# Optimization experiments

Measured on AMD Instinct MI355X. Metric: run time of the kernel, lower is better.

## Reference

```python
import jax, jax.numpy as jnp
import numpy as np

E = 8          # num_experts
K = 2          # top_k
CAPF = 1.25    # capacity_factor
DIM = 512
HID = 2048     # int(dim * mlp_ratio)


def setup_inputs() -> dict:
    key = jax.random.key(0)
    ks = jax.random.split(key, 5)
    s = 0.02
    x = jax.random.normal(ks[0], (8, 2048, DIM), jnp.float32)
    Wr = jax.random.normal(ks[1], (E, DIM), jnp.float32) * s          # router weight (no bias)
    W1 = jax.random.normal(ks[2], (E, HID, DIM), jnp.float32) * s     # fc1 weights per expert
    b1 = jnp.zeros((E, HID), jnp.float32)
    W2 = jax.random.normal(ks[3], (E, DIM, HID), jnp.float32) * s     # fc2 weights per expert
    b2 = jnp.zeros((E, DIM), jnp.float32)
    return {"x": x, "Wr": Wr, "W1": W1, "b1": b1, "W2": W2, "b2": b2}


def _capacity_keep(top_w, top_idx, cap):
    """For each (slot, expert), keep only the `cap` highest-weight tokens.
    top_w, top_idx: [T, K]. Returns bool keep mask [T, K]."""
    def per_slot(w, idx):
        order = jnp.argsort(-w)                       # tokens sorted by weight desc
        idx_sorted = idx[order]                       # [T] expert id in sorted order
        oh = jax.nn.one_hot(idx_sorted, E, dtype=jnp.int32)
        rank = jnp.cumsum(oh, axis=0) - 1             # rank within each expert
        r = jnp.take_along_axis(rank, idx_sorted[:, None], axis=1)[:, 0]
        keep_sorted = r < cap
        return jnp.zeros(w.shape[0], bool).at[order].set(keep_sorted)
    return jax.vmap(per_slot, in_axes=(1, 1), out_axes=1)(top_w, top_idx)


def reference(x, Wr, W1, b1, W2, b2):
    b, n, d = x.shape
    T = b * n
    flat = x.reshape(T, d)

    # Router: softmax in fp32 then cast back
    logits = flat @ Wr.T                                            # [T, E]
    probs = jax.nn.softmax(logits.astype(jnp.float32), axis=-1).astype(flat.dtype)
    top_w, top_idx = jax.lax.top_k(probs, K)                        # [T, K]
    top_w = top_w / (jnp.sum(top_w, axis=-1, keepdims=True) + 1e-8)

    # Capacity-limited drop, then renormalize
    cap = max(1, int(CAPF * T * K / E))
    keep = _capacity_keep(top_w, top_idx, cap)
    top_w = jnp.where(keep, top_w, 0.0)
    top_w = top_w / jnp.clip(jnp.sum(top_w, axis=-1, keepdims=True), 1e-8, None)

    # Combine weight per (token, expert): scatter-add top_w into dense [T, E]
    rows = jnp.arange(T)[:, None]
    w_te = jnp.zeros((T, E), flat.dtype).at[rows, top_idx].add(top_w)

    # Per-expert MLP, weighted combine (w_te is 0 for unassigned/dropped pairs)
    out = jnp.zeros_like(flat)
    for e in range(E):
        h = jax.nn.gelu(flat @ W1[e].T + b1[e], approximate=False)  # [T, HID]
        y = h @ W2[e].T + b2[e]                                     # [T, D]
        out = out + w_te[:, e:e + 1] * y

    # Load-balancing aux loss
    load = jnp.sum(w_te, axis=0) / T
    importance = probs.mean(0)
    aux = jnp.sum(importance * load * float(E))
    return out.reshape(b, n, d), aux
```

## Files before the change

### kernel.cpp

```cpp
#include <hip/hip_runtime.h>
#include <hip/hip_bf16.h>
#include <math.h>

#define DIM 512
#define HID 2048
#define NE  8
#define CSTRIDE 32
#define CVTB 1024

typedef __attribute__((ext_vector_type(8))) short short8;
typedef __attribute__((ext_vector_type(4))) float f32x4;
typedef unsigned short ushort_t;

static __device__ __forceinline__ ushort_t f2bf(float f) {
    unsigned int x = __builtin_bit_cast(unsigned int, f);
    unsigned int lsb = (x >> 16) & 1u;
    x += 0x7fffu + lsb;
    return (ushort_t)(x >> 16);
}
static __device__ __forceinline__ float bf2f(ushort_t u) {
    unsigned int x = ((unsigned int)u) << 16;
    return __builtin_bit_cast(float, x);
}

static __device__ __forceinline__ float fast_gelu(float v) {
    float z = v * fmaf(0.071354816f, v * v, 1.5957691f);
    return v * __builtin_amdgcn_rcpf(1.f + __expf(-z));
}

static __device__ __forceinline__ void gld16(const void* g, void* l) {
    __builtin_amdgcn_global_load_lds(
        (const __attribute__((address_space(1))) void*)g,
        (__attribute__((address_space(3))) void*)l,
        16, 0, 0);
}

__global__ __launch_bounds__(256) void k_init(
    const float* __restrict__ W1, ushort_t* __restrict__ W1b, int n1,
    const float* __restrict__ W2, ushort_t* __restrict__ W2b, int n2,
    const float* __restrict__ x, const float* __restrict__ Wr,
    ushort_t* __restrict__ xb, float* __restrict__ probs,
    int* __restrict__ tidx, float* __restrict__ tw, int T)
{
    if (blockIdx.x < CVTB) {
        int i = blockIdx.x * 256 + threadIdx.x;
        int stride = CVTB * 256;
        int n4a = n1 >> 2, n4b = n2 >> 2;
        for (int j = i; j < n4a; j += stride) {
            float4 v = ((const float4*)W1)[j];
            ushort4 o;
            o.x = f2bf(v.x); o.y = f2bf(v.y); o.z = f2bf(v.z); o.w = f2bf(v.w);
            ((ushort4*)W1b)[j] = o;
        }
        for (int j = i; j < n4b; j += stride) {
            float4 v = ((const float4*)W2)[j];
            ushort4 o;
            o.x = f2bf(v.x); o.y = f2bf(v.y); o.z = f2bf(v.z); o.w = f2bf(v.w);
            ((ushort4*)W2b)[j] = o;
        }
        return;
    }
    int lane = threadIdx.x & 63;
    int t = (blockIdx.x - CVTB) * 4 + (threadIdx.x >> 6);
    if (t >= T) return;
    const float* xr = x + (size_t)t * DIM;
    double acc[NE];
#pragma unroll
    for (int e = 0; e < NE; e++) acc[e] = 0.0;
    for (int i = lane; i < DIM; i += 64) {
        float xv = xr[i];
        xb[(size_t)t * DIM + i] = f2bf(xv);
        double xd = (double)xv;
#pragma unroll
        for (int e = 0; e < NE; e++) acc[e] += xd * (double)Wr[e * DIM + i];
    }
#pragma unroll
    for (int e = 0; e < NE; e++) {
#pragma unroll
        for (int off = 32; off > 0; off >>= 1) acc[e] += __shfl_xor(acc[e], off);
    }
    double mx = acc[0];
#pragma unroll
    for (int e = 1; e < NE; e++) mx = fmax(mx, acc[e]);
    double p[NE], sum = 0.0;
#pragma unroll
    for (int e = 0; e < NE; e++) { p[e] = exp(acc[e] - mx); sum += p[e]; }
    float pr[NE];
#pragma unroll
    for (int e = 0; e < NE; e++) pr[e] = (float)(p[e] / sum);
    if (lane < NE) probs[(size_t)t * NE + lane] = pr[lane];
    if (lane == 0) {
        int i1 = 0; float b1v = pr[0];
#pragma unroll
        for (int e = 1; e < NE; e++) if (pr[e] > b1v) { b1v = pr[e]; i1 = e; }
        int i2 = -1; float b2v = -1.f;
#pragma unroll
        for (int e = 0; e < NE; e++) if (e != i1 && pr[e] > b2v) { b2v = pr[e]; i2 = e; }
        float s2 = b1v + b2v + 1e-8f;
        tidx[t * 2] = i1; tidx[t * 2 + 1] = i2;
        tw[t * 2] = b1v / s2; tw[t * 2 + 1] = b2v / s2;
    }
}

__global__ __launch_bounds__(256) void k_hist(const int* __restrict__ tidx,
                                              int* __restrict__ cnt, int T) {
    __shared__ int h[16];
    if (threadIdx.x < 16) h[threadIdx.x] = 0;
    __syncthreads();
    int stride = gridDim.x * blockDim.x;
    for (int t = blockIdx.x * blockDim.x + threadIdx.x; t < T; t += stride) {
        atomicAdd(&h[tidx[t * 2]], 1);
        atomicAdd(&h[8 + tidx[t * 2 + 1]], 1);
    }
    __syncthreads();
    if (threadIdx.x < 16 && h[threadIdx.x] != 0)
        atomicAdd(&cnt[threadIdx.x * CSTRIDE], h[threadIdx.x]);
}

__global__ __launch_bounds__(256) void k_post(const int* __restrict__ tidx,
        const float* __restrict__ tw, const int* __restrict__ cnt,
        const float* __restrict__ probs, int* __restrict__ lcnt,
        int* __restrict__ ltok, int* __restrict__ pos, float* __restrict__ tw2,
        float* __restrict__ partial, int T, int cap, int capM)
{
    __shared__ int h[NE];
    __shared__ int base[NE];
    __shared__ float red[256 * 16];
    if (threadIdx.x < NE) h[threadIdx.x] = 0;
    __syncthreads();
    int t = blockIdx.x * blockDim.x + threadIdx.x;
    float wkn[2] = {0.f, 0.f};
    int myE[2] = {-1, -1};
    int myp[2] = {0, 0};
    if (t < T) {
        float wk[2]; int es[2];
#pragma unroll
        for (int s = 0; s < 2; s++) {
            int e = tidx[t * 2 + s];
            float w = tw[t * 2 + s];
            es[s] = e; wk[s] = w;
            if (cnt[(s * NE + e) * CSTRIDE] > cap) {
                int rank = 0;
                for (int t2 = 0; t2 < T; t2++) {
                    if (tidx[t2 * 2 + s] == e) {
                        float w2 = tw[t2 * 2 + s];
                        if (w2 > w || (w2 == w && t2 < t)) rank++;
                    }
                }
                if (rank >= cap) wk[s] = 0.f;
            }
        }
        float denom = fmaxf(wk[0] + wk[1], 1e-8f);
#pragma unroll
        for (int s = 0; s < 2; s++) {
            wkn[s] = wk[s] / denom;
            tw2[t * 2 + s] = wkn[s];
            if (wkn[s] != 0.f) {
                myE[s] = es[s];
                myp[s] = atomicAdd(&h[es[s]], 1);
            }
        }
    }
    __syncthreads();
    if (threadIdx.x < NE)
        base[threadIdx.x] = (h[threadIdx.x] != 0)
            ? atomicAdd(&lcnt[threadIdx.x * CSTRIDE], h[threadIdx.x]) : 0;
    __syncthreads();
    float imp[NE], ld[NE];
#pragma unroll
    for (int e = 0; e < NE; e++) { imp[e] = 0.f; ld[e] = 0.f; }
    if (t < T) {
#pragma unroll
        for (int s = 0; s < 2; s++) {
            if (myE[s] >= 0) {
                int p = base[myE[s]] + myp[s];
                ltok[myE[s] * capM + p] = t;
                pos[t * 2 + s] = (myE[s] << 20) | p;
                ld[myE[s]] += wkn[s];
            } else {
                pos[t * 2 + s] = -1;
            }
        }
#pragma unroll
        for (int e = 0; e < NE; e++) imp[e] = probs[(size_t)t * NE + e];
    }
#pragma unroll
    for (int e = 0; e < NE; e++) {
        red[threadIdx.x * 16 + e] = imp[e];
        red[threadIdx.x * 16 + 8 + e] = ld[e];
    }
    __syncthreads();
    for (int off = 128; off > 0; off >>= 1) {
        if (threadIdx.x < off) {
#pragma unroll
            for (int j = 0; j < 16; j++)
                red[threadIdx.x * 16 + j] += red[(threadIdx.x + off) * 16 + j];
        }
        __syncthreads();
    }
    if (threadIdx.x < 16) partial[blockIdx.x * 16 + threadIdx.x] = red[threadIdx.x];
}

__global__ void k_tail(const int* __restrict__ lcnt, int* __restrict__ loff,
                       const float* __restrict__ partial, float* __restrict__ outaux,
                       int nb, int T)
{
    __shared__ float s[16];
    if (threadIdx.x == 0) {
        int o = 0;
        for (int e = 0; e < NE; e++) {
            loff[e] = o;
            o += ((lcnt[e * CSTRIDE] + 127) >> 7) << 7;
        }
        loff[NE] = o;
    }
    if (threadIdx.x < 16) {
        float a = 0.f;
        for (int b = 0; b < nb; b++) a += partial[b * 16 + threadIdx.x];
        s[threadIdx.x] = a;
    }
    __syncthreads();
    if (threadIdx.x == 0) {
        float invT = 1.f / (float)T;
        float aux = 0.f;
        for (int e = 0; e < NE; e++)
            aux += (s[e] * invT) * (s[8 + e] * invT) * (float)NE;
        outaux[0] = aux;
    }
}

__global__ __launch_bounds__(256, 2) void k_fc1(
    const ushort_t* __restrict__ xb, const ushort_t* __restrict__ W1b,
    const float* __restrict__ b1, const int* __restrict__ lcnt,
    const int* __restrict__ loff, const int* __restrict__ ltok,
    ushort_t* __restrict__ hbuf, int capM)
{
    int bx = blockIdx.x;
    int e  = bx & 7;
    int r  = bx >> 3;
    int mt = r >> 4;
    int nt = r & 15;
    int cnt = lcnt[e * CSTRIDE];
    if (cnt > capM) cnt = capM;
    int m0 = mt * 128;
    if (m0 >= cnt) return;
    int n0 = nt * 128;
    const int* toks = ltok + e * capM;
    int hrow0 = loff[e] + m0;
    const ushort_t* Bsrc = W1b + (size_t)e * HID * DIM;

    __shared__ char smem[65536];
    char* As0 = smem;          char* Bs0 = smem + 16384;
    char* As1 = smem + 32768;  char* Bs1 = smem + 49152;

    int tid = threadIdx.x;
    int wave = tid >> 6, lane = tid & 63;
    int wm = wave >> 1, wn = wave & 1;

    const char* aSrc[4]; const char* bSrc[4]; int ldst[4];
#pragma unroll
    for (int i = 0; i < 4; i++) {
        int c = tid + 256 * i;
        int row = c >> 3, cc = c & 7;
        int scc = cc ^ (row & 7);
        int gr = m0 + row;
        int tok = toks[gr < cnt ? gr : (cnt - 1)];
        aSrc[i] = (const char*)(xb + (size_t)tok * DIM + scc * 8);
        bSrc[i] = (const char*)(Bsrc + (size_t)(n0 + row) * DIM + scc * 8);
        ldst[i] = (i * 256 + wave * 64) * 16;
    }

    f32x4 acc[4][4];
#pragma unroll
    for (int a = 0; a < 4; a++)
#pragma unroll
        for (int b = 0; b < 4; b++) acc[a][b] = (f32x4){0.f, 0.f, 0.f, 0.f};

    int aRow = wm * 64 + (lane & 15);
    int bRow = wn * 64 + (lane & 15);
    int kq = lane >> 4;
    int swz0 = (kq ^ (lane & 7)) << 4;
    int swz1 = ((4 + kq) ^ (lane & 7)) << 4;
    int aoff[2] = { aRow * 128 + swz0, aRow * 128 + swz1 };
    int boff[2] = { bRow * 128 + swz0, bRow * 128 + swz1 };

    auto STAGE = [&](int kofs, char* A, char* B) {
#pragma unroll
        for (int i = 0; i < 4; i++) {
            gld16(aSrc[i] + kofs, A + ldst[i]);
            gld16(bSrc[i] + kofs, B + ldst[i]);
        }
    };
    auto COMPUTE = [&](const char* A, const char* B) {
#pragma unroll
        for (int kk = 0; kk < 2; kk++) {
            short8 af[4], bfr[4];
#pragma unroll
            for (int mf = 0; mf < 4; mf++)
                af[mf] = *(const short8*)(A + aoff[kk] + mf * 2048);
#pragma unroll
            for (int nf = 0; nf < 4; nf++)
                bfr[nf] = *(const short8*)(B + boff[kk] + nf * 2048);
#pragma unroll
            for (int mf = 0; mf < 4; mf++)
#pragma unroll
                for (int nf = 0; nf < 4; nf++)
                    acc[mf][nf] = __builtin_amdgcn_mfma_f32_16x16x32_bf16(bfr[nf], af[mf], acc[mf][nf], 0, 0, 0);
        }
    };

    const int NT = DIM / 64;
    STAGE(0, As0, Bs0);
#pragma unroll
    for (int t = 0; t < NT; t++) {
        char* Ac = (t & 1) ? As1 : As0;
        char* Bc = (t & 1) ? Bs1 : Bs0;
        if (t + 1 < NT) {
            STAGE((t + 1) * 128, (t & 1) ? As0 : As1, (t & 1) ? Bs0 : Bs1);
            asm volatile("s_waitcnt vmcnt(8)" ::: "memory");
        } else {
            asm volatile("s_waitcnt vmcnt(0)" ::: "memory");
        }
        __builtin_amdgcn_s_barrier();
        __builtin_amdgcn_sched_barrier(0);
        COMPUTE(Ac, Bc);
        __builtin_amdgcn_sched_barrier(0);
        __builtin_amdgcn_s_barrier();
    }

    const float* b1e = b1 + e * HID;
    int mlocal = wm * 64 + (lane & 15);
    int nbase0 = n0 + wn * 64 + (lane >> 4) * 4;
#pragma unroll
    for (int mf = 0; mf < 4; mf++) {
        int mrow = mlocal + mf * 16;
        bool valid = (m0 + mrow) < cnt;
        ushort_t* dst = hbuf + (size_t)(hrow0 + mrow) * HID;
#pragma unroll
        for (int nf = 0; nf < 4; nf++) {
            int nc = nbase0 + nf * 16;
            float4 bias4 = *(const float4*)(b1e + nc);
            ushort4 o;
            o.x = f2bf(fast_gelu(acc[mf][nf][0] + bias4.x));
            o.y = f2bf(fast_gelu(acc[mf][nf][1] + bias4.y));
            o.z = f2bf(fast_gelu(acc[mf][nf][2] + bias4.z));
            o.w = f2bf(fast_gelu(acc[mf][nf][3] + bias4.w));
            if (valid) *(ushort4*)(dst + nc) = o;
        }
    }
}

__global__ __launch_bounds__(256, 2) void k_fc2(
    const ushort_t* __restrict__ hbuf, const ushort_t* __restrict__ W2b,
    const float* __restrict__ b2, const int* __restrict__ lcnt,
    const int* __restrict__ loff, ushort_t* __restrict__ ybuf, int capM)
{
    int bx = blockIdx.x;
    int e  = bx & 7;
    int r  = bx >> 3;
    int mt = r >> 2;
    int nt = r & 3;
    int cnt = lcnt[e * CSTRIDE];
    if (cnt > capM) cnt = capM;
    int m0 = mt * 128;
    if (m0 >= cnt) return;
    int n0 = nt * 128;
    int hrow0 = loff[e] + m0;
    const ushort_t* Bsrc = W2b + (size_t)e * DIM * HID;

    __shared__ char smem[65536];
    char* As0 = smem;          char* Bs0 = smem + 16384;
    char* As1 = smem + 32768;  char* Bs1 = smem + 49152;

    int tid = threadIdx.x;
    int wave = tid >> 6, lane = tid & 63;
    int wm = wave >> 1, wn = wave & 1;

    const char* aSrc[4]; const char* bSrc[4]; int ldst[4];
#pragma unroll
    for (int i = 0; i < 4; i++) {
        int c = tid + 256 * i;
        int row = c >> 3, cc = c & 7;
        int scc = cc ^ (row & 7);
        aSrc[i] = (const char*)(hbuf + (size_t)(hrow0 + row) * HID + scc * 8);
        bSrc[i] = (const char*)(Bsrc + (size_t)(n0 + row) * HID + scc * 8);
        ldst[i] = (i * 256 + wave * 64) * 16;
    }

    f32x4 acc[4][4];
#pragma unroll
    for (int a = 0; a < 4; a++)
#pragma unroll
        for (int b = 0; b < 4; b++) acc[a][b] = (f32x4){0.f, 0.f, 0.f, 0.f};

    int aRow = wm * 64 + (lane & 15);
    int bRow = wn * 64 + (lane & 15);
    int kq = lane >> 4;
    int swz0 = (kq ^ (lane & 7)) << 4;
    int swz1 = ((4 + kq) ^ (lane & 7)) << 4;
    int aoff[2] = { aRow * 128 + swz0, aRow * 128 + swz1 };
    int boff[2] = { bRow * 128 + swz0, bRow * 128 + swz1 };

    auto STAGE = [&](int kofs, char* A, char* B) {
#pragma unroll
        for (int i = 0; i < 4; i++) {
            gld16(aSrc[i] + kofs, A + ldst[i]);
            gld16(bSrc[i] + kofs, B + ldst[i]);
        }
    };
    auto COMPUTE = [&](const char* A, const char* B) {
#pragma unroll
        for (int kk = 0; kk < 2; kk++) {
            short8 af[4], bfr[4];
#pragma unroll
            for (int mf = 0; mf < 4; mf++)
                af[mf] = *(const short8*)(A + aoff[kk] + mf * 2048);
#pragma unroll
            for (int nf = 0; nf < 4; nf++)
                bfr[nf] = *(const short8*)(B + boff[kk] + nf * 2048);
#pragma unroll
            for (int mf = 0; mf < 4; mf++)
#pragma unroll
                for (int nf = 0; nf < 4; nf++)
                    acc[mf][nf] = __builtin_amdgcn_mfma_f32_16x16x32_bf16(bfr[nf], af[mf], acc[mf][nf], 0, 0, 0);
        }
    };

    const int NT = HID / 64;
    STAGE(0, As0, Bs0);
#pragma unroll
    for (int t = 0; t < NT; t++) {
        char* Ac = (t & 1) ? As1 : As0;
        char* Bc = (t & 1) ? Bs1 : Bs0;
        if (t + 1 < NT) {
            STAGE((t + 1) * 128, (t & 1) ? As0 : As1, (t & 1) ? Bs0 : Bs1);
            asm volatile("s_waitcnt vmcnt(8)" ::: "memory");
        } else {
            asm volatile("s_waitcnt vmcnt(0)" ::: "memory");
        }
        __builtin_amdgcn_s_barrier();
        __builtin_amdgcn_sched_barrier(0);
        COMPUTE(Ac, Bc);
        __builtin_amdgcn_sched_barrier(0);
        __builtin_amdgcn_s_barrier();
    }

    const float* b2e = b2 + e * DIM;
    int mlocal = wm * 64 + (lane & 15);
    int nbase0 = n0 + wn * 64 + (lane >> 4) * 4;
#pragma unroll
    for (int mf = 0; mf < 4; mf++) {
        int mrow = mlocal + mf * 16;
        bool valid = (m0 + mrow) < cnt;
        ushort_t* dst = ybuf + (size_t)(hrow0 + mrow) * DIM;
#pragma unroll
        for (int nf = 0; nf < 4; nf++) {
            int nc = nbase0 + nf * 16;
            float4 bias4 = *(const float4*)(b2e + nc);
            ushort4 o;
            o.x = f2bf(acc[mf][nf][0] + bias4.x);
            o.y = f2bf(acc[mf][nf][1] + bias4.y);
            o.z = f2bf(acc[mf][nf][2] + bias4.z);
            o.w = f2bf(acc[mf][nf][3] + bias4.w);
            if (valid) *(ushort4*)(dst + nc) = o;
        }
    }
}

__global__ __launch_bounds__(256) void k_comb(const ushort_t* __restrict__ ybuf,
    const float* __restrict__ tw2, const int* __restrict__ pos,
    const int* __restrict__ loff, float* __restrict__ out, int T, int capM)
{
    int wv = threadIdx.x >> 6, lane = threadIdx.x & 63;
    int t = blockIdx.x * 4 + wv;
    if (t >= T) return;
    float o[8];
#pragma unroll
    for (int j = 0; j < 8; j++) o[j] = 0.f;
#pragma unroll
    for (int s = 0; s < 2; s++) {
        int pk = pos[t * 2 + s];
        if (pk >= 0) {
            float w = tw2[t * 2 + s];
            int e = pk >> 20, p = pk & 0xFFFFF;
            int row = loff[e] + p;
            short8 y = *(const short8*)(ybuf + (size_t)row * DIM + lane * 8);
#pragma unroll
            for (int j = 0; j < 8; j++) o[j] += w * bf2f((ushort_t)y[j]);
        }
    }
    float4* dst = (float4*)(out + (size_t)t * DIM + lane * 8);
    dst[0] = (float4){o[0], o[1], o[2], o[3]};
    dst[1] = (float4){o[4], o[5], o[6], o[7]};
}

extern "C" void kernel_launch(void* const* d_in, const int* in_sizes, int n_in,
                              void* d_out, int out_size, void* d_ws, size_t ws_size,
                              hipStream_t stream)
{
    const float* x  = (const float*)d_in[0];
    const float* Wr = (const float*)d_in[1];
    const float* W1 = (const float*)d_in[2];
    const float* b1 = (const float*)d_in[3];
    const float* W2 = (const float*)d_in[4];
    const float* b2 = (const float*)d_in[5];
    float* out = (float*)d_out;

    int T = in_sizes[0] / DIM;
    int cap = (int)(1.25 * (double)T * 2.0 / 8.0);
    if (cap < 1) cap = 1;
    int capM = 2 * cap; if (capM > T) capM = T;
    int mtmax = (capM + 127) / 128;
    int nposts = (T + 255) / 256;

    char* w = (char*)d_ws;
    size_t off = 0;
    auto alloc = [&](size_t bytes) {
        char* p = w + off;
        off = (off + bytes + 255) & ~(size_t)255;
        return p;
    };
    size_t ybrows = (size_t)T * 2 + NE * 128;
    size_t ybbytes = ybrows * DIM * 2;
    ushort_t* ybuf = (ushort_t*)w;
    ushort_t* xb   = (ushort_t*)alloc((size_t)T * DIM * 2);
    ushort_t* W1b  = (ushort_t*)alloc((size_t)NE * HID * DIM * 2);
    if (off < ybbytes) off = (ybbytes + 255) & ~(size_t)255;
    ushort_t* W2b  = (ushort_t*)alloc((size_t)NE * DIM * HID * 2);
    ushort_t* hbuf = (ushort_t*)alloc(ybrows * HID * 2);
    float* probs   = (float*)alloc((size_t)T * NE * 4);
    int*   tidx    = (int*)alloc((size_t)T * 2 * 4);
    float* tw      = (float*)alloc((size_t)T * 2 * 4);
    float* tw2     = (float*)alloc((size_t)T * 2 * 4);
    int*   pos     = (int*)alloc((size_t)T * 2 * 4);
    int*   cnt     = (int*)alloc(16 * CSTRIDE * 4);
    int*   lcnt    = (int*)alloc(NE * CSTRIDE * 4);
    int*   loff    = (int*)alloc((NE + 1) * 4);
    int*   ltok    = (int*)alloc((size_t)NE * capM * 4);
    float* partial = (float*)alloc((size_t)nposts * 16 * 4);

    (void)hipMemsetAsync(cnt, 0, 16 * CSTRIDE * 4, stream);
    (void)hipMemsetAsync(lcnt, 0, NE * CSTRIDE * 4, stream);

    int nrb = (T + 3) / 4;
    k_init<<<CVTB + nrb, 256, 0, stream>>>(W1, W1b, NE * HID * DIM,
                                           W2, W2b, NE * DIM * HID,
                                           x, Wr, xb, probs, tidx, tw, T);
    k_hist<<<64, 256, 0, stream>>>(tidx, cnt, T);
    k_post<<<nposts, 256, 0, stream>>>(tidx, tw, cnt, probs, lcnt, ltok, pos, tw2,
                                       partial, T, cap, capM);
    k_tail<<<1, 64, 0, stream>>>(lcnt, loff, partial, out + (size_t)T * DIM, nposts, T);

    k_fc1<<<NE * mtmax * (HID / 128), 256, 0, stream>>>(
        xb, W1b, b1, lcnt, loff, ltok, hbuf, capM);
    k_fc2<<<NE * mtmax * (DIM / 128), 256, 0, stream>>>(
        hbuf, W2b, b2, lcnt, loff, ybuf, capM);
    k_comb<<<(T + 3) / 4, 256, 0, stream>>>(ybuf, tw2, pos, loff, out, T, capM);
}
```

Baseline: 267.3 us.

## Enlarge expert GEMM tiles to 256x256 with 8 waves and interleaved MFMA phases

Moves the fc1 and fc2 grouped GEMMs from 128x128 tiles with 4 waves to 256x256 tiles with 8 waves. Each wave now holds 128x64 accumulators, and the kernels use 128KB of dynamic LDS for double buffering. The inner loop is split into four phases separated by barriers, with s_setprio raised around the MFMA bursts so waves interleave LDS reads and matrix math. Expert segment padding grows to 256 rows. The aim is more operand reuse per LDS load, at the cost of higher register pressure, fewer blocks per CU, and more padded wasted rows for small expert counts.

```diff
diff --git a/kernel.cpp b/kernel.cpp
--- a/kernel.cpp
+++ b/kernel.cpp
@@ -34,6 +34,19 @@
         (__attribute__((address_space(3))) void*)l,
         16, 0, 0);
 }
+
+#define LOADB4(Bb, KK) { _Pragma("unroll") \
+    for (int nf = 0; nf < 4; nf++) \
+        bfr[nf] = *(const short8*)((Bb) + boff[KK] + nf * 2048); }
+#define LOADA4(Ab, KK, MH) { _Pragma("unroll") \
+    for (int j = 0; j < 4; j++) \
+        af[j] = *(const short8*)((Ab) + aoff[KK] + ((MH) * 4 + j) * 2048); }
+#define MFMA16(MH) { __builtin_amdgcn_s_setprio(1); _Pragma("unroll") \
+    for (int j = 0; j < 4; j++) { _Pragma("unroll") \
+        for (int nf = 0; nf < 4; nf++) \
+            acc[(MH) * 4 + j][nf] = __builtin_amdgcn_mfma_f32_16x16x32_bf16( \
+                bfr[nf], af[j], acc[(MH) * 4 + j][nf], 0, 0, 0); } \
+    __builtin_amdgcn_s_setprio(0); }
 
 __global__ __launch_bounds__(256) void k_init(
     const float* __restrict__ W1, ushort_t* __restrict__ W1b, int n1,
@@ -210,7 +223,7 @@
         int o = 0;
         for (int e = 0; e < NE; e++) {
             loff[e] = o;
-            o += ((lcnt[e * CSTRIDE] + 127) >> 7) << 7;
+            o += ((lcnt[e * CSTRIDE] + 255) >> 8) << 8;
         }
         loff[NE] = o;
     }
@@ -229,54 +242,54 @@
     }
 }
 
-__global__ __launch_bounds__(256, 2) void k_fc1(
+__global__ __launch_bounds__(512, 2) void k_fc1(
     const ushort_t* __restrict__ xb, const ushort_t* __restrict__ W1b,
     const float* __restrict__ b1, const int* __restrict__ lcnt,
     const int* __restrict__ loff, const int* __restrict__ ltok,
     ushort_t* __restrict__ hbuf, int capM)
 {
+    extern __shared__ char smem[];
     int bx = blockIdx.x;
     int e  = bx & 7;
     int r  = bx >> 3;
-    int mt = r >> 4;
-    int nt = r & 15;
+    int mt = r >> 3;
+    int nt = r & 7;
     int cnt = lcnt[e * CSTRIDE];
     if (cnt > capM) cnt = capM;
-    int m0 = mt * 128;
+    int m0 = mt * 256;
     if (m0 >= cnt) return;
-    int n0 = nt * 128;
+    int n0 = nt * 256;
     const int* toks = ltok + e * capM;
     int hrow0 = loff[e] + m0;
     const ushort_t* Bsrc = W1b + (size_t)e * HID * DIM;
 
-    __shared__ char smem[65536];
-    char* As0 = smem;          char* Bs0 = smem + 16384;
-    char* As1 = smem + 32768;  char* Bs1 = smem + 49152;
+    char* A0 = smem;          char* A1 = smem + 32768;
+    char* B0 = smem + 65536;  char* B1 = smem + 98304;
 
     int tid = threadIdx.x;
     int wave = tid >> 6, lane = tid & 63;
-    int wm = wave >> 1, wn = wave & 1;
+    int wm = wave >> 2, wn = wave & 3;
 
     const char* aSrc[4]; const char* bSrc[4]; int ldst[4];
 #pragma unroll
     for (int i = 0; i < 4; i++) {
-        int c = tid + 256 * i;
+        int c = tid + 512 * i;
         int row = c >> 3, cc = c & 7;
         int scc = cc ^ (row & 7);
         int gr = m0 + row;
         int tok = toks[gr < cnt ? gr : (cnt - 1)];
         aSrc[i] = (const char*)(xb + (size_t)tok * DIM + scc * 8);
         bSrc[i] = (const char*)(Bsrc + (size_t)(n0 + row) * DIM + scc * 8);
-        ldst[i] = (i * 256 + wave * 64) * 16;
-    }
-
-    f32x4 acc[4][4];
-#pragma unroll
-    for (int a = 0; a < 4; a++)
+        ldst[i] = (wave * 64 + 512 * i) * 16;
+    }
+
+    f32x4 acc[8][4];
+#pragma unroll
+    for (int a = 0; a < 8; a++)
 #pragma unroll
         for (int b = 0; b < 4; b++) acc[a][b] = (f32x4){0.f, 0.f, 0.f, 0.f};
 
-    int aRow = wm * 64 + (lane & 15);
+    int aRow = wm * 128 + (lane & 15);
     int bRow = wn * 64 + (lane & 15);
     int kq = lane >> 4;
     int swz0 = (kq ^ (lane & 7)) << 4;
@@ -291,48 +304,41 @@
             gld16(bSrc[i] + kofs, B + ldst[i]);
         }
     };
-    auto COMPUTE = [&](const char* A, const char* B) {
-#pragma unroll
-        for (int kk = 0; kk < 2; kk++) {
-            short8 af[4], bfr[4];
-#pragma unroll
-            for (int mf = 0; mf < 4; mf++)
-                af[mf] = *(const short8*)(A + aoff[kk] + mf * 2048);
-#pragma unroll
-            for (int nf = 0; nf < 4; nf++)
-                bfr[nf] = *(const short8*)(B + boff[kk] + nf * 2048);
-#pragma unroll
-            for (int mf = 0; mf < 4; mf++)
-#pragma unroll
-                for (int nf = 0; nf < 4; nf++)
-                    acc[mf][nf] = __builtin_amdgcn_mfma_f32_16x16x32_bf16(bfr[nf], af[mf], acc[mf][nf], 0, 0, 0);
-        }
-    };
 
     const int NT = DIM / 64;
-    STAGE(0, As0, Bs0);
-#pragma unroll
+    STAGE(0, A0, B0);
+    asm volatile("s_waitcnt vmcnt(0)" ::: "memory");
+    __builtin_amdgcn_s_barrier();
+    char *Ac = A0, *Bc = B0, *An = A1, *Bn = B1;
     for (int t = 0; t < NT; t++) {
-        char* Ac = (t & 1) ? As1 : As0;
-        char* Bc = (t & 1) ? Bs1 : Bs0;
         if (t + 1 < NT) {
-            STAGE((t + 1) * 128, (t & 1) ? As0 : As1, (t & 1) ? Bs0 : Bs1);
+            STAGE((t + 1) * 128, An, Bn);
             asm volatile("s_waitcnt vmcnt(8)" ::: "memory");
         } else {
             asm volatile("s_waitcnt vmcnt(0)" ::: "memory");
         }
         __builtin_amdgcn_s_barrier();
         __builtin_amdgcn_sched_barrier(0);
-        COMPUTE(Ac, Bc);
-        __builtin_amdgcn_sched_barrier(0);
-        __builtin_amdgcn_s_barrier();
+        {
+            short8 af[4], bfr[4];
+            LOADB4(Bc, 0); LOADA4(Ac, 0, 0); MFMA16(0);
+            __builtin_amdgcn_s_barrier();
+            LOADA4(Ac, 0, 1); MFMA16(1);
+            __builtin_amdgcn_s_barrier();
+            LOADB4(Bc, 1); LOADA4(Ac, 1, 0); MFMA16(0);
+            __builtin_amdgcn_s_barrier();
+            LOADA4(Ac, 1, 1); MFMA16(1);
+            __builtin_amdgcn_s_barrier();
+        }
+        char* ta = Ac; Ac = An; An = ta;
+        char* tb = Bc; Bc = Bn; Bn = tb;
     }
 
     const float* b1e = b1 + e * HID;
-    int mlocal = wm * 64 + (lane & 15);
+    int mlocal = wm * 128 + (lane & 15);
     int nbase0 = n0 + wn * 64 + (lane >> 4) * 4;
 #pragma unroll
-    for (int mf = 0; mf < 4; mf++) {
+    for (int mf = 0; mf < 8; mf++) {
         int mrow = mlocal + mf * 16;
         bool valid = (m0 + mrow) < cnt;
         ushort_t* dst = hbuf + (size_t)(hrow0 + mrow) * HID;
@@ -350,50 +356,50 @@
     }
 }
 
-__global__ __launch_bounds__(256, 2) void k_fc2(
+__global__ __launch_bounds__(512, 2) void k_fc2(
     const ushort_t* __restrict__ hbuf, const ushort_t* __restrict__ W2b,
     const float* __restrict__ b2, const int* __restrict__ lcnt,
     const int* __restrict__ loff, ushort_t* __restrict__ ybuf, int capM)
 {
+    extern __shared__ char smem[];
     int bx = blockIdx.x;
     int e  = bx & 7;
     int r  = bx >> 3;
-    int mt = r >> 2;
-    int nt = r & 3;
+    int mt = r >> 1;
+    int nt = r & 1;
     int cnt = lcnt[e * CSTRIDE];
     if (cnt > capM) cnt = capM;
-    int m0 = mt * 128;
+    int m0 = mt * 256;
     if (m0 >= cnt) return;
-    int n0 = nt * 128;
+    int n0 = nt * 256;
     int hrow0 = loff[e] + m0;
     const ushort_t* Bsrc = W2b + (size_t)e * DIM * HID;
 
-    __shared__ char smem[65536];
-    char* As0 = smem;          char* Bs0 = smem + 16384;
-    char* As1 = smem + 32768;  char* Bs1 = smem + 49152;
+    char* A0 = smem;          char* A1 = smem + 32768;
+    char* B0 = smem + 65536;  char* B1 = smem + 98304;
 
     int tid = threadIdx.x;
     int wave = tid >> 6, lane = tid & 63;
-    int wm = wave >> 1, wn = wave & 1;
+    int wm = wave >> 2, wn = wave & 3;
 
     const char* aSrc[4]; const char* bSrc[4]; int ldst[4];
 #pragma unroll
     for (int i = 0; i < 4; i++) {
-        int c = tid + 256 * i;
+        int c = tid + 512 * i;
         int row = c >> 3, cc = c & 7;
         int scc = cc ^ (row & 7);
         aSrc[i] = (const char*)(hbuf + (size_t)(hrow0 + row) * HID + scc * 8);
         bSrc[i] = (const char*)(Bsrc + (size_t)(n0 + row) * HID + scc * 8);
-        ldst[i] = (i * 256 + wave * 64) * 16;
-    }
-
-    f32x4 acc[4][4];
-#pragma unroll
-    for (int a = 0; a < 4; a++)
+        ldst[i] = (wave * 64 + 512 * i) * 16;
+    }
+
+    f32x4 acc[8][4];
+#pragma unroll
+    for (int a = 0; a < 8; a++)
 #pragma unroll
         for (int b = 0; b < 4; b++) acc[a][b] = (f32x4){0.f, 0.f, 0.f, 0.f};
 
-    int aRow = wm * 64 + (lane & 15);
+    int aRow = wm * 128 + (lane & 15);
     int bRow = wn * 64 + (lane & 15);
     int kq = lane >> 4;
     int swz0 = (kq ^ (lane & 7)) << 4;
@@ -408,48 +414,41 @@
             gld16(bSrc[i] + kofs, B + ldst[i]);
         }
     };
-    auto COMPUTE = [&](const char* A, const char* B) {
-#pragma unroll
-        for (int kk = 0; kk < 2; kk++) {
-            short8 af[4], bfr[4];
-#pragma unroll
-            for (int mf = 0; mf < 4; mf++)
-                af[mf] = *(const short8*)(A + aoff[kk] + mf * 2048);
-#pragma unroll
-            for (int nf = 0; nf < 4; nf++)
-                bfr[nf] = *(const short8*)(B + boff[kk] + nf * 2048);
-#pragma unroll
-            for (int mf = 0; mf < 4; mf++)
-#pragma unroll
-                for (int nf = 0; nf < 4; nf++)
-                    acc[mf][nf] = __builtin_amdgcn_mfma_f32_16x16x32_bf16(bfr[nf], af[mf], acc[mf][nf], 0, 0, 0);
-        }
-    };
 
     const int NT = HID / 64;
-    STAGE(0, As0, Bs0);
-#pragma unroll
+    STAGE(0, A0, B0);
+    asm volatile("s_waitcnt vmcnt(0)" ::: "memory");
+    __builtin_amdgcn_s_barrier();
+    char *Ac = A0, *Bc = B0, *An = A1, *Bn = B1;
     for (int t = 0; t < NT; t++) {
-        char* Ac = (t & 1) ? As1 : As0;
-        char* Bc = (t & 1) ? Bs1 : Bs0;
         if (t + 1 < NT) {
-            STAGE((t + 1) * 128, (t & 1) ? As0 : As1, (t & 1) ? Bs0 : Bs1);
+            STAGE((t + 1) * 128, An, Bn);
             asm volatile("s_waitcnt vmcnt(8)" ::: "memory");
         } else {
             asm volatile("s_waitcnt vmcnt(0)" ::: "memory");
         }
         __builtin_amdgcn_s_barrier();
         __builtin_amdgcn_sched_barrier(0);
-        COMPUTE(Ac, Bc);
-        __builtin_amdgcn_sched_barrier(0);
-        __builtin_amdgcn_s_barrier();
+        {
+            short8 af[4], bfr[4];
+            LOADB4(Bc, 0); LOADA4(Ac, 0, 0); MFMA16(0);
+            __builtin_amdgcn_s_barrier();
+            LOADA4(Ac, 0, 1); MFMA16(1);
+            __builtin_amdgcn_s_barrier();
+            LOADB4(Bc, 1); LOADA4(Ac, 1, 0); MFMA16(0);
+            __builtin_amdgcn_s_barrier();
+            LOADA4(Ac, 1, 1); MFMA16(1);
+            __builtin_amdgcn_s_barrier();
+        }
+        char* ta = Ac; Ac = An; An = ta;
+        char* tb = Bc; Bc = Bn; Bn = tb;
     }
 
     const float* b2e = b2 + e * DIM;
-    int mlocal = wm * 64 + (lane & 15);
+    int mlocal = wm * 128 + (lane & 15);
     int nbase0 = n0 + wn * 64 + (lane >> 4) * 4;
 #pragma unroll
-    for (int mf = 0; mf < 4; mf++) {
+    for (int mf = 0; mf < 8; mf++) {
         int mrow = mlocal + mf * 16;
         bool valid = (m0 + mrow) < cnt;
         ushort_t* dst = ybuf + (size_t)(hrow0 + mrow) * DIM;
@@ -510,8 +509,13 @@
     int cap = (int)(1.25 * (double)T * 2.0 / 8.0);
     if (cap < 1) cap = 1;
     int capM = 2 * cap; if (capM > T) capM = T;
-    int mtmax = (capM + 127) / 128;
+    int mtmax = (capM + 255) / 256;
     int nposts = (T + 255) / 256;
+
+    (void)hipFuncSetAttribute((const void*)k_fc1,
+        hipFuncAttributeMaxDynamicSharedMemorySize, 131072);
+    (void)hipFuncSetAttribute((const void*)k_fc2,
+        hipFuncAttributeMaxDynamicSharedMemorySize, 131072);
 
     char* w = (char*)d_ws;
     size_t off = 0;
@@ -520,7 +524,7 @@
         off = (off + bytes + 255) & ~(size_t)255;
         return p;
     };
-    size_t ybrows = (size_t)T * 2 + NE * 128;
+    size_t ybrows = (size_t)T * 2 + NE * 256;
     size_t ybbytes = ybrows * DIM * 2;
     ushort_t* ybuf = (ushort_t*)w;
     ushort_t* xb   = (ushort_t*)alloc((size_t)T * DIM * 2);
@@ -551,9 +555,9 @@
                                        partial, T, cap, capM);
     k_tail<<<1, 64, 0, stream>>>(lcnt, loff, partial, out + (size_t)T * DIM, nposts, T);
 
-    k_fc1<<<NE * mtmax * (HID / 128), 256, 0, stream>>>(
+    k_fc1<<<NE * mtmax * (HID / 256), 512, 131072, stream>>>(
         xb, W1b, b1, lcnt, loff, ltok, hbuf, capM);
-    k_fc2<<<NE * mtmax * (DIM / 128), 256, 0, stream>>>(
+    k_fc2<<<NE * mtmax * (DIM / 256), 512, 131072, stream>>>(
         hbuf, W2b, b2, lcnt, loff, ybuf, capM);
     k_comb<<<(T + 3) / 4, 256, 0, stream>>>(ybuf, tw2, pos, loff, out, T, capM);
 }
```

New measurement: 337.7 us. 26.4% more time.
